# Kernel tuning notes

Measured on AMD Instinct MI355X. Metric: run time of the kernel, lower is better.

The kernel has to match this reference:

```python
import jax, jax.numpy as jnp
import numpy as np

NEG_SLOPE = 0.2  # PyG GATConv default

def gat_conv(x, src, dst, W, att_src, att_dst, bias, n_nodes):
    """PyG-style GATConv (self-loops already included in src/dst)."""
    H, C = att_src.shape
    h = (x @ W).reshape(n_nodes, H, C)                       # [N,H,C]
    a_src = jnp.einsum('nhc,hc->nh', h, att_src)             # [N,H]
    a_dst = jnp.einsum('nhc,hc->nh', h, att_dst)             # [N,H]
    e = jax.nn.leaky_relu(a_src[src] + a_dst[dst], NEG_SLOPE)  # [E,H]
    # numerically stable segment softmax over incoming edges of each dst node
    e_max = jax.ops.segment_max(e, dst, num_segments=n_nodes)   # [N,H]
    e_exp = jnp.exp(e - e_max[dst])
    denom = jax.ops.segment_sum(e_exp, dst, num_segments=n_nodes)  # [N,H]
    alpha = e_exp / (denom[dst] + 1e-16)                     # [E,H]
    msg = h[src] * alpha[:, :, None]                         # [E,H,C]
    out = jax.ops.segment_sum(msg, dst, num_segments=n_nodes)  # [N,H,C]
    return out.reshape(n_nodes, H * C) + bias

def add_self_loops(edge_index, n_nodes):
    loop = jnp.arange(n_nodes, dtype=edge_index.dtype)
    src = jnp.concatenate([edge_index[0], loop])
    dst = jnp.concatenate([edge_index[1], loop])
    return src, dst

def setup_inputs() -> dict:
    key = jax.random.key(0)
    ks = jax.random.split(key, 12)
    N, E, IN, HID, H1 = 50000, 800000, 128, 64, 4
    s = lambda k, shape, scale: jax.random.normal(k, shape, dtype=jnp.float32) * scale
    return {
        'x': s(ks[0], (N, IN), 1.0),
        'edge_index': jax.random.randint(ks[1], (2, E), 0, N, dtype=jnp.int64),
        'W1': s(ks[2], (IN, H1 * HID), (2.0 / IN) ** 0.5),
        'att_src1': s(ks[3], (H1, HID), 0.1),
        'att_dst1': s(ks[4], (H1, HID), 0.1),
        'b1': s(ks[5], (H1 * HID,), 0.02),
        'W2': s(ks[6], (H1 * HID, HID), (2.0 / (H1 * HID)) ** 0.5),
        'att_src2': s(ks[7], (1, HID), 0.1),
        'att_dst2': s(ks[8], (1, HID), 0.1),
        'b2': s(ks[9], (HID,), 0.02),
        'Ws': s(ks[10], (HID, 1), (2.0 / HID) ** 0.5),
        'bs': s(ks[11], (1,), 0.02),
    }

def reference(x, edge_index, W1, att_src1, att_dst1, b1, W2, att_src2, att_dst2, b2, Ws, bs):
    N = x.shape[0]
    src, dst = add_self_loops(edge_index, N)
    h = jax.nn.elu(gat_conv(x, src, dst, W1, att_src1, att_dst1, b1, N))   # [N,256]
    # dropout is identity in eval mode
    h = jax.nn.elu(gat_conv(h, src, dst, W2, att_src2, att_dst2, b2, N))   # [N,64]
    scores = (h @ Ws + bs).squeeze(-1)                                     # [N]
    return h, scores
```

## Files before the change

kernel.cpp:

```cpp
#include <hip/hip_runtime.h>
#include <hip/hip_bf16.h>
#include <math.h>


#define LRELU_SLOPE 0.2f

typedef __attribute__((ext_vector_type(8))) short short8;
typedef __attribute__((ext_vector_type(4))) float f32x4;

__device__ inline ushort f2bf(float f) {
    uint u = __float_as_uint(f);
    return (ushort)((u + 0x7FFFu + ((u >> 16) & 1u)) >> 16);
}
__device__ inline float bf2f(ushort u) {
    return __uint_as_float(((uint)u) << 16);
}

__global__ __launch_bounds__(256)
void prefrag(const float* __restrict__ W, ushort* __restrict__ out,
             int J, int T, int ldn)
{
    int tid = blockIdx.x * blockDim.x + threadIdx.x;
    if (tid >= J * T * 64) return;
    int l = tid & 63, jt = tid >> 6;
    int t = jt % T, j = jt / T;
    int n = j * 16 + (l & 15);
    int k0 = t * 32 + (l >> 4) * 8;
    ushort o[8];
    #pragma unroll
    for (int b = 0; b < 8; ++b) o[b] = f2bf(W[(size_t)(k0 + b) * ldn + n]);
    *(short8*)(out + (size_t)tid * 8) = *(short8*)o;
}

template<int J, int T, int H, bool AF32>
__global__ __launch_bounds__(256)
void gemm_mfma(const void* __restrict__ Araw, const ushort* __restrict__ Bf,
               ushort* __restrict__ Cbf, const float* __restrict__ attS,
               const float* __restrict__ attD, float* __restrict__ as_,
               float* __restrict__ ad_, int M)
{
    constexpr int K = 32 * T;
    constexpr int NN = 16 * J;
    const int l = threadIdx.x & 63;
    const int wid = blockIdx.x * (blockDim.x >> 6) + (threadIdx.x >> 6);
    const int base = wid * 16;
    if (base >= M) return;
    const int lm = l & 15, lg = l >> 4;

    short8 a[T];
    if constexpr (AF32) {
        const float* ap = (const float*)Araw + (size_t)(base + lm) * K + lg * 8;
        #pragma unroll
        for (int t = 0; t < T; ++t) {
            float4 v0 = *(const float4*)(ap + t * 32);
            float4 v1 = *(const float4*)(ap + t * 32 + 4);
            ushort o[8];
            o[0] = f2bf(v0.x); o[1] = f2bf(v0.y); o[2] = f2bf(v0.z); o[3] = f2bf(v0.w);
            o[4] = f2bf(v1.x); o[5] = f2bf(v1.y); o[6] = f2bf(v1.z); o[7] = f2bf(v1.w);
            a[t] = *(short8*)o;
        }
    } else {
        const ushort* ap = (const ushort*)Araw + (size_t)(base + lm) * K + lg * 8;
        #pragma unroll
        for (int t = 0; t < T; ++t) a[t] = *(const short8*)(ap + t * 32);
    }

    f32x4 acc[J];
    #pragma unroll
    for (int j = 0; j < J; ++j) acc[j] = (f32x4){0.f, 0.f, 0.f, 0.f};

    const ushort* bp = Bf + (size_t)l * 8;
    #pragma unroll
    for (int j = 0; j < J; ++j)
        #pragma unroll
        for (int t = 0; t < T; ++t) {
            short8 b = *(const short8*)(bp + (size_t)(j * T + t) * 512);
            acc[j] = __builtin_amdgcn_mfma_f32_16x16x32_bf16(a[t], b, acc[j], 0, 0, 0);
        }

    float sp[H][4], dp[H][4];
    #pragma unroll
    for (int h = 0; h < H; ++h)
        #pragma unroll
        for (int r = 0; r < 4; ++r) { sp[h][r] = 0.f; dp[h][r] = 0.f; }

    #pragma unroll
    for (int j = 0; j < J; ++j) {
        const int h = j / (J / H);
        const int coff = (j % (J / H)) * 16 + lm;
        float ws = attS[h * 64 + coff];
        float wd = attD[h * 64 + coff];
        #pragma unroll
        for (int r = 0; r < 4; ++r) {
            int row = base + lg * 4 + r;
            Cbf[(size_t)row * NN + j * 16 + lm] = f2bf(acc[j][r]);
            sp[h][r] = fmaf(acc[j][r], ws, sp[h][r]);
            dp[h][r] = fmaf(acc[j][r], wd, dp[h][r]);
        }
    }
    #pragma unroll
    for (int h = 0; h < H; ++h)
        #pragma unroll
        for (int r = 0; r < 4; ++r) {
            float s = sp[h][r], d = dp[h][r];
            s += __shfl_xor(s, 1); d += __shfl_xor(d, 1);
            s += __shfl_xor(s, 2); d += __shfl_xor(d, 2);
            s += __shfl_xor(s, 4); d += __shfl_xor(d, 4);
            s += __shfl_xor(s, 8); d += __shfl_xor(d, 8);
            if (lm == 0) {
                int row = base + lg * 4 + r;
                as_[row * H + h] = s;
                ad_[row * H + h] = d;
            }
        }
}

__global__ __launch_bounds__(256)
void degree_hist(const int* __restrict__ edst, int* __restrict__ deg, int E)
{
    int i = blockIdx.x * blockDim.x + threadIdx.x;
    if (i < E) atomicAdd(&deg[edst[i]], 1);
}

__global__ __launch_bounds__(1024)
void scan_rowptr(const int* __restrict__ deg, int* __restrict__ rowptr,
                 int* __restrict__ cursor, int N)
{
    __shared__ int wsums[16];
    __shared__ int s_carry;
    const int tid = threadIdx.x, lane = tid & 63, wid = tid >> 6;
    if (tid == 0) s_carry = 0;
    __syncthreads();
    const int N4 = N >> 2;
    for (int base = 0; base < N4; base += 1024) {
        int i4 = base + tid;
        int4 v = (i4 < N4) ? ((const int4*)deg)[i4] : make_int4(0, 0, 0, 0);
        int tsum = v.x + v.y + v.z + v.w;
        int sc = tsum;
        #pragma unroll
        for (int off = 1; off < 64; off <<= 1) {
            int t = __shfl_up(sc, off);
            if (lane >= off) sc += t;
        }
        if (lane == 63) wsums[wid] = sc;
        __syncthreads();
        if (wid == 0) {
            int wv = (lane < 16) ? wsums[lane] : 0;
            #pragma unroll
            for (int off = 1; off < 16; off <<= 1) {
                int t = __shfl_up(wv, off);
                if (lane >= off) wv += t;
            }
            if (lane < 16) wsums[lane] = wv;
        }
        __syncthreads();
        int wbase = (wid > 0) ? wsums[wid - 1] : 0;
        int excl = s_carry + wbase + sc - tsum;
        if (i4 < N4) {
            int4 o;
            o.x = excl; o.y = excl + v.x; o.z = o.y + v.y; o.w = o.z + v.z;
            ((int4*)rowptr)[i4] = o;
            ((int4*)cursor)[i4] = make_int4(0, 0, 0, 0);
        }
        __syncthreads();
        if (tid == 0) s_carry += wsums[15];
        __syncthreads();
    }
    if (tid == 0) rowptr[N] = s_carry;
}

__global__ __launch_bounds__(256)
void scatter_edges(const int* __restrict__ esrc, const int* __restrict__ edst,
                   const int* __restrict__ rowptr, int* __restrict__ cursor,
                   int* __restrict__ csr_src, int* __restrict__ csr_dst, int E)
{
    int i = blockIdx.x * blockDim.x + threadIdx.x;
    if (i >= E) return;
    int s = esrc[i], d = edst[i];
    int pos = rowptr[d] + atomicAdd(&cursor[d], 1);
    csr_src[pos] = s;
    csr_dst[pos] = d;
}

__global__ __launch_bounds__(256)
void edge_coef_l1(const int* __restrict__ csr_src, const int* __restrict__ csr_dst,
                  const float* __restrict__ as_, const float* __restrict__ ad_,
                  float* __restrict__ p1, int E)
{
    int i = blockIdx.x * blockDim.x + threadIdx.x;
    if (i >= E) return;
    int s = csr_src[i], d = csr_dst[i];
    float4 a = *(const float4*)(as_ + (size_t)s * 4);
    float4 b = *(const float4*)(ad_ + (size_t)d * 4);
    float4 o;
    float e0 = a.x + b.x; e0 = e0 > 0.f ? e0 : LRELU_SLOPE * e0; o.x = __expf(e0);
    float e1 = a.y + b.y; e1 = e1 > 0.f ? e1 : LRELU_SLOPE * e1; o.y = __expf(e1);
    float e2 = a.z + b.z; e2 = e2 > 0.f ? e2 : LRELU_SLOPE * e2; o.z = __expf(e2);
    float e3 = a.w + b.w; e3 = e3 > 0.f ? e3 : LRELU_SLOPE * e3; o.w = __expf(e3);
    *(float4*)(p1 + (size_t)i * 4) = o;
}

__global__ __launch_bounds__(256)
void edge_coef_l2(const int* __restrict__ csr_src, const int* __restrict__ csr_dst,
                  const float* __restrict__ as_, const float* __restrict__ ad_,
                  float* __restrict__ p2, int E)
{
    int i = blockIdx.x * blockDim.x + threadIdx.x;
    if (i >= E) return;
    float e0 = as_[csr_src[i]] + ad_[csr_dst[i]];
    e0 = e0 > 0.f ? e0 : LRELU_SLOPE * e0;
    p2[i] = __expf(e0);
}

__global__ __launch_bounds__(256)
void aggregate_l1(const int* __restrict__ rowptr, const int* __restrict__ csr_src,
                  const float* __restrict__ p1, const ushort* __restrict__ h1,
                  const float* __restrict__ as_, const float* __restrict__ ad_,
                  const float* __restrict__ bias, ushort* __restrict__ outbf, int N)
{
    int w = (blockIdx.x * blockDim.x + threadIdx.x) >> 6;
    int lane = threadIdx.x & 63;
    if (w >= N) return;
    const int head = lane >> 4;
    const int c0 = lane << 2;
    float4 acc;
    float dsum;

    {
        float el = as_[w * 4 + head] + ad_[w * 4 + head];
        el = el > 0.f ? el : LRELU_SLOPE * el;
        float p = __expf(el);
        ushort4 u = *(const ushort4*)(h1 + (size_t)w * 256 + c0);
        acc.x = p * bf2f(u.x); acc.y = p * bf2f(u.y);
        acc.z = p * bf2f(u.z); acc.w = p * bf2f(u.w);
        dsum = p;
    }

    int e = rowptr[w];
    const int e1 = rowptr[w + 1];
    for (; e + 3 < e1; e += 4) {
        int s0 = csr_src[e],     s1 = csr_src[e + 1];
        int s2 = csr_src[e + 2], s3 = csr_src[e + 3];
        float p0 = p1[(size_t)(e + 0) * 4 + head];
        float p1v = p1[(size_t)(e + 1) * 4 + head];
        float p2 = p1[(size_t)(e + 2) * 4 + head];
        float p3 = p1[(size_t)(e + 3) * 4 + head];
        ushort4 u0 = *(const ushort4*)(h1 + (size_t)s0 * 256 + c0);
        ushort4 u1 = *(const ushort4*)(h1 + (size_t)s1 * 256 + c0);
        ushort4 u2 = *(const ushort4*)(h1 + (size_t)s2 * 256 + c0);
        ushort4 u3 = *(const ushort4*)(h1 + (size_t)s3 * 256 + c0);
        acc.x = fmaf(p0, bf2f(u0.x), acc.x); acc.y = fmaf(p0, bf2f(u0.y), acc.y);
        acc.z = fmaf(p0, bf2f(u0.z), acc.z); acc.w = fmaf(p0, bf2f(u0.w), acc.w);
        acc.x = fmaf(p1v, bf2f(u1.x), acc.x); acc.y = fmaf(p1v, bf2f(u1.y), acc.y);
        acc.z = fmaf(p1v, bf2f(u1.z), acc.z); acc.w = fmaf(p1v, bf2f(u1.w), acc.w);
        acc.x = fmaf(p2, bf2f(u2.x), acc.x); acc.y = fmaf(p2, bf2f(u2.y), acc.y);
        acc.z = fmaf(p2, bf2f(u2.z), acc.z); acc.w = fmaf(p2, bf2f(u2.w), acc.w);
        acc.x = fmaf(p3, bf2f(u3.x), acc.x); acc.y = fmaf(p3, bf2f(u3.y), acc.y);
        acc.z = fmaf(p3, bf2f(u3.z), acc.z); acc.w = fmaf(p3, bf2f(u3.w), acc.w);
        dsum += (p0 + p1v) + (p2 + p3);
    }
    for (; e < e1; ++e) {
        int s0 = csr_src[e];
        float p0 = p1[(size_t)e * 4 + head];
        ushort4 u0 = *(const ushort4*)(h1 + (size_t)s0 * 256 + c0);
        acc.x = fmaf(p0, bf2f(u0.x), acc.x); acc.y = fmaf(p0, bf2f(u0.y), acc.y);
        acc.z = fmaf(p0, bf2f(u0.z), acc.z); acc.w = fmaf(p0, bf2f(u0.w), acc.w);
        dsum += p0;
    }
    const float inv = 1.f / (dsum + 1e-16f);
    const float4 b = *(const float4*)(bias + c0);
    float ox = acc.x * inv + b.x; ox = ox > 0.f ? ox : expm1f(ox);
    float oy = acc.y * inv + b.y; oy = oy > 0.f ? oy : expm1f(oy);
    float oz = acc.z * inv + b.z; oz = oz > 0.f ? oz : expm1f(oz);
    float ow = acc.w * inv + b.w; ow = ow > 0.f ? ow : expm1f(ow);
    ushort4 o;
    o.x = f2bf(ox); o.y = f2bf(oy); o.z = f2bf(oz); o.w = f2bf(ow);
    *(ushort4*)(outbf + (size_t)w * 256 + c0) = o;
}

__global__ __launch_bounds__(256)
void aggregate_l2(const int* __restrict__ rowptr, const int* __restrict__ csr_src,
                  const float* __restrict__ p2, const ushort* __restrict__ h2,
                  const float* __restrict__ as_, const float* __restrict__ ad_,
                  const float* __restrict__ b2, const float* __restrict__ Wsv,
                  const float* __restrict__ bs, float* __restrict__ hout,
                  float* __restrict__ scores, int N)
{
    int w = (blockIdx.x * blockDim.x + threadIdx.x) >> 6;
    int lane = threadIdx.x & 63;
    if (w >= N) return;
    float acc, dsum;
    {
        float el = as_[w] + ad_[w];
        el = el > 0.f ? el : LRELU_SLOPE * el;
        float p = __expf(el);
        acc = p * bf2f(h2[(size_t)w * 64 + lane]);
        dsum = p;
    }
    int e = rowptr[w];
    const int e1 = rowptr[w + 1];
    for (; e + 3 < e1; e += 4) {
        int s0 = csr_src[e],     s1 = csr_src[e + 1];
        int s2 = csr_src[e + 2], s3 = csr_src[e + 3];
        float p0 = p2[e], p1 = p2[e + 1], p2v = p2[e + 2], p3 = p2[e + 3];
        acc = fmaf(p0, bf2f(h2[(size_t)s0 * 64 + lane]), acc);
        acc = fmaf(p1, bf2f(h2[(size_t)s1 * 64 + lane]), acc);
        acc = fmaf(p2v, bf2f(h2[(size_t)s2 * 64 + lane]), acc);
        acc = fmaf(p3, bf2f(h2[(size_t)s3 * 64 + lane]), acc);
        dsum += (p0 + p1) + (p2v + p3);
    }
    for (; e < e1; ++e) {
        int s0 = csr_src[e];
        float p0 = p2[e];
        acc = fmaf(p0, bf2f(h2[(size_t)s0 * 64 + lane]), acc);
        dsum += p0;
    }
    float v = acc / (dsum + 1e-16f) + b2[lane];
    v = v > 0.f ? v : expm1f(v);
    hout[(size_t)w * 64 + lane] = v;
    float sc = v * Wsv[lane];
    #pragma unroll
    for (int off = 32; off; off >>= 1) sc += __shfl_down(sc, off);
    if (lane == 0) scores[w] = sc + bs[0];
}

extern "C" void kernel_launch(void* const* d_in, const int* in_sizes, int n_in,
                              void* d_out, int out_size, void* d_ws, size_t ws_size,
                              hipStream_t stream)
{
    const float* x    = (const float*)d_in[0];
    const int*   ei   = (const int*)d_in[1];
    const float* W1   = (const float*)d_in[2];
    const float* as1w = (const float*)d_in[3];
    const float* ad1w = (const float*)d_in[4];
    const float* b1   = (const float*)d_in[5];
    const float* W2   = (const float*)d_in[6];
    const float* as2w = (const float*)d_in[7];
    const float* ad2w = (const float*)d_in[8];
    const float* b2   = (const float*)d_in[9];
    const float* Ws   = (const float*)d_in[10];
    const float* bs   = (const float*)d_in[11];

    const int N  = in_sizes[0] / 128;
    const int E  = in_sizes[1] / 2;
    const int* esrc = ei;
    const int* edst = ei + E;

    ushort* h1bf  = (ushort*)d_ws;
    ushort* hl1bf = h1bf + (size_t)N * 256;
    ushort* h2bf  = hl1bf + (size_t)N * 256;
    ushort* bfr1  = h2bf + (size_t)N * 64;
    ushort* bfr2  = bfr1 + 32768;
    float*  as1   = (float*)(bfr2 + 16384);
    float*  ad1   = as1 + (size_t)N * 4;
    float*  as2   = ad1 + (size_t)N * 4;
    float*  ad2   = as2 + N;
    float*  p1    = ad2 + N;
    float*  p2    = p1 + (size_t)E * 4;
    int*    deg    = (int*)(p2 + E);
    int*    cursor = deg + N;
    int*    rowptr = cursor + N;
    int*    csr_src= rowptr + N + 4;
    int*    csr_dst= csr_src + E;

    float* hout   = (float*)d_out;
    float* scores = hout + (size_t)N * 64;

    hipMemsetAsync(deg, 0, (size_t)N * sizeof(int), stream);
    degree_hist<<<(E + 255) / 256, 256, 0, stream>>>(edst, deg, E);
    scan_rowptr<<<1, 1024, 0, stream>>>(deg, rowptr, cursor, N);
    scatter_edges<<<(E + 255) / 256, 256, 0, stream>>>(
        esrc, edst, rowptr, cursor, csr_src, csr_dst, E);

    prefrag<<<(16 * 4 * 64 + 255) / 256, 256, 0, stream>>>(W1, bfr1, 16, 4, 256);
    prefrag<<<(4 * 8 * 64 + 255) / 256, 256, 0, stream>>>(W2, bfr2, 4, 8, 64);

    gemm_mfma<16, 4, 4, true><<<(N / 16 + 3) / 4, 256, 0, stream>>>(
        x, bfr1, h1bf, as1w, ad1w, as1, ad1, N);
    edge_coef_l1<<<(E + 255) / 256, 256, 0, stream>>>(
        csr_src, csr_dst, as1, ad1, p1, E);
    aggregate_l1<<<((size_t)N * 64 + 255) / 256, 256, 0, stream>>>(
        rowptr, csr_src, p1, h1bf, as1, ad1, b1, hl1bf, N);

    gemm_mfma<4, 8, 1, false><<<(N / 16 + 3) / 4, 256, 0, stream>>>(
        hl1bf, bfr2, h2bf, as2w, ad2w, as2, ad2, N);
    edge_coef_l2<<<(E + 255) / 256, 256, 0, stream>>>(
        csr_src, csr_dst, as2, ad2, p2, E);
    aggregate_l2<<<((size_t)N * 64 + 255) / 256, 256, 0, stream>>>(
        rowptr, csr_src, p2, h2bf, as2, ad2, b2, Ws, bs, hout, scores, N);
}
```

Baseline: 266.2 us.

## Split wavefront across multiple edges per iteration in GAT aggregation kernels

Both aggregation kernels now process several incoming edges at once per wavefront. The lanes are split into half-waves (layer 1, 16-byte loads per lane) or quarter-waves (layer 2, 8-byte loads), each handling a different edge, and the partial sums are combined with cross-lane shuffles at the end. The goal is more independent gathers in flight and wider per-lane loads, to hide gather latency on short adjacency lists. In exchange, the tail iterations do masked, redundant loads, the shuffle reductions add overhead, and some lanes do duplicate epilogue work.

```diff
diff --git a/kernel.cpp b/kernel.cpp
--- a/kernel.cpp
+++ b/kernel.cpp
@@ -221,61 +221,60 @@
     int w = (blockIdx.x * blockDim.x + threadIdx.x) >> 6;
     int lane = threadIdx.x & 63;
     if (w >= N) return;
-    const int head = lane >> 4;
-    const int c0 = lane << 2;
-    float4 acc;
+    const int half = lane >> 5;
+    const int hl   = lane & 31;
+    const int c0   = hl << 3;
+    const int head = hl >> 3;
+
+    float acc[8];
     float dsum;
-
     {
         float el = as_[w * 4 + head] + ad_[w * 4 + head];
         el = el > 0.f ? el : LRELU_SLOPE * el;
-        float p = __expf(el);
-        ushort4 u = *(const ushort4*)(h1 + (size_t)w * 256 + c0);
-        acc.x = p * bf2f(u.x); acc.y = p * bf2f(u.y);
-        acc.z = p * bf2f(u.z); acc.w = p * bf2f(u.w);
+        float p = half ? 0.f : __expf(el);
+        ushort u8[8];
+        *(short8*)u8 = *(const short8*)(h1 + (size_t)w * 256 + c0);
+        #pragma unroll
+        for (int k = 0; k < 8; ++k) acc[k] = p * bf2f(u8[k]);
         dsum = p;
     }
 
     int e = rowptr[w];
     const int e1 = rowptr[w + 1];
-    for (; e + 3 < e1; e += 4) {
-        int s0 = csr_src[e],     s1 = csr_src[e + 1];
-        int s2 = csr_src[e + 2], s3 = csr_src[e + 3];
-        float p0 = p1[(size_t)(e + 0) * 4 + head];
-        float p1v = p1[(size_t)(e + 1) * 4 + head];
-        float p2 = p1[(size_t)(e + 2) * 4 + head];
-        float p3 = p1[(size_t)(e + 3) * 4 + head];
-        ushort4 u0 = *(const ushort4*)(h1 + (size_t)s0 * 256 + c0);
-        ushort4 u1 = *(const ushort4*)(h1 + (size_t)s1 * 256 + c0);
-        ushort4 u2 = *(const ushort4*)(h1 + (size_t)s2 * 256 + c0);
-        ushort4 u3 = *(const ushort4*)(h1 + (size_t)s3 * 256 + c0);
-        acc.x = fmaf(p0, bf2f(u0.x), acc.x); acc.y = fmaf(p0, bf2f(u0.y), acc.y);
-        acc.z = fmaf(p0, bf2f(u0.z), acc.z); acc.w = fmaf(p0, bf2f(u0.w), acc.w);
-        acc.x = fmaf(p1v, bf2f(u1.x), acc.x); acc.y = fmaf(p1v, bf2f(u1.y), acc.y);
-        acc.z = fmaf(p1v, bf2f(u1.z), acc.z); acc.w = fmaf(p1v, bf2f(u1.w), acc.w);
-        acc.x = fmaf(p2, bf2f(u2.x), acc.x); acc.y = fmaf(p2, bf2f(u2.y), acc.y);
-        acc.z = fmaf(p2, bf2f(u2.z), acc.z); acc.w = fmaf(p2, bf2f(u2.w), acc.w);
-        acc.x = fmaf(p3, bf2f(u3.x), acc.x); acc.y = fmaf(p3, bf2f(u3.y), acc.y);
-        acc.z = fmaf(p3, bf2f(u3.z), acc.z); acc.w = fmaf(p3, bf2f(u3.w), acc.w);
-        dsum += (p0 + p1v) + (p2 + p3);
-    }
-    for (; e < e1; ++e) {
-        int s0 = csr_src[e];
-        float p0 = p1[(size_t)e * 4 + head];
-        ushort4 u0 = *(const ushort4*)(h1 + (size_t)s0 * 256 + c0);
-        acc.x = fmaf(p0, bf2f(u0.x), acc.x); acc.y = fmaf(p0, bf2f(u0.y), acc.y);
-        acc.z = fmaf(p0, bf2f(u0.z), acc.z); acc.w = fmaf(p0, bf2f(u0.w), acc.w);
-        dsum += p0;
-    }
+    const int eL = e1 - 1;
+    while (e < e1) {
+        #pragma unroll
+        for (int u = 0; u < 4; ++u) {
+            int m = e + 2 * u + half;
+            int idx = m <= eL ? m : eL;
+            int s = csr_src[idx];
+            float p = m <= eL ? p1[(size_t)idx * 4 + head] : 0.f;
+            ushort u8[8];
+            *(short8*)u8 = *(const short8*)(h1 + (size_t)s * 256 + c0);
+            #pragma unroll
+            for (int k = 0; k < 8; ++k) acc[k] = fmaf(p, bf2f(u8[k]), acc[k]);
+            dsum += p;
+        }
+        e += 8;
+    }
+
+    dsum += __shfl_xor(dsum, 32);
+    #pragma unroll
+    for (int k = 0; k < 8; ++k) acc[k] += __shfl_xor(acc[k], 32);
+
     const float inv = 1.f / (dsum + 1e-16f);
-    const float4 b = *(const float4*)(bias + c0);
-    float ox = acc.x * inv + b.x; ox = ox > 0.f ? ox : expm1f(ox);
-    float oy = acc.y * inv + b.y; oy = oy > 0.f ? oy : expm1f(oy);
-    float oz = acc.z * inv + b.z; oz = oz > 0.f ? oz : expm1f(oz);
-    float ow = acc.w * inv + b.w; ow = ow > 0.f ? ow : expm1f(ow);
-    ushort4 o;
-    o.x = f2bf(ox); o.y = f2bf(oy); o.z = f2bf(oz); o.w = f2bf(ow);
-    *(ushort4*)(outbf + (size_t)w * 256 + c0) = o;
+    const float4 b0 = *(const float4*)(bias + c0);
+    const float4 b1 = *(const float4*)(bias + c0 + 4);
+    float bb[8] = {b0.x, b0.y, b0.z, b0.w, b1.x, b1.y, b1.z, b1.w};
+    ushort o[8];
+    #pragma unroll
+    for (int k = 0; k < 8; ++k) {
+        float v = acc[k] * inv + bb[k];
+        v = v > 0.f ? v : expm1f(v);
+        o[k] = f2bf(v);
+    }
+    if (half == 0)
+        *(short8*)(outbf + (size_t)w * 256 + c0) = *(short8*)o;
 }
 
 __global__ __launch_bounds__(256)
@@ -289,38 +288,61 @@
     int w = (blockIdx.x * blockDim.x + threadIdx.x) >> 6;
     int lane = threadIdx.x & 63;
     if (w >= N) return;
-    float acc, dsum;
+    const int q  = lane >> 4;
+    const int ql = lane & 15;
+    const int c0 = ql << 2;
+
+    float acc[4];
+    float dsum;
     {
         float el = as_[w] + ad_[w];
         el = el > 0.f ? el : LRELU_SLOPE * el;
-        float p = __expf(el);
-        acc = p * bf2f(h2[(size_t)w * 64 + lane]);
+        float p = (q == 0) ? __expf(el) : 0.f;
+        ushort u4[4];
+        *(ushort4*)u4 = *(const ushort4*)(h2 + (size_t)w * 64 + c0);
+        #pragma unroll
+        for (int k = 0; k < 4; ++k) acc[k] = p * bf2f(u4[k]);
         dsum = p;
     }
+
     int e = rowptr[w];
     const int e1 = rowptr[w + 1];
-    for (; e + 3 < e1; e += 4) {
-        int s0 = csr_src[e],     s1 = csr_src[e + 1];
-        int s2 = csr_src[e + 2], s3 = csr_src[e + 3];
-        float p0 = p2[e], p1 = p2[e + 1], p2v = p2[e + 2], p3 = p2[e + 3];
-        acc = fmaf(p0, bf2f(h2[(size_t)s0 * 64 + lane]), acc);
-        acc = fmaf(p1, bf2f(h2[(size_t)s1 * 64 + lane]), acc);
-        acc = fmaf(p2v, bf2f(h2[(size_t)s2 * 64 + lane]), acc);
-        acc = fmaf(p3, bf2f(h2[(size_t)s3 * 64 + lane]), acc);
-        dsum += (p0 + p1) + (p2v + p3);
-    }
-    for (; e < e1; ++e) {
-        int s0 = csr_src[e];
-        float p0 = p2[e];
-        acc = fmaf(p0, bf2f(h2[(size_t)s0 * 64 + lane]), acc);
-        dsum += p0;
-    }
-    float v = acc / (dsum + 1e-16f) + b2[lane];
-    v = v > 0.f ? v : expm1f(v);
-    hout[(size_t)w * 64 + lane] = v;
-    float sc = v * Wsv[lane];
-    #pragma unroll
-    for (int off = 32; off; off >>= 1) sc += __shfl_down(sc, off);
+    const int eL = e1 - 1;
+    while (e < e1) {
+        #pragma unroll
+        for (int u = 0; u < 2; ++u) {
+            int m = e + 4 * u + q;
+            int idx = m <= eL ? m : eL;
+            int s = csr_src[idx];
+            float p = m <= eL ? p2[idx] : 0.f;
+            ushort u4[4];
+            *(ushort4*)u4 = *(const ushort4*)(h2 + (size_t)s * 64 + c0);
+            #pragma unroll
+            for (int k = 0; k < 4; ++k) acc[k] = fmaf(p, bf2f(u4[k]), acc[k]);
+            dsum += p;
+        }
+        e += 8;
+    }
+
+    dsum += __shfl_xor(dsum, 16); dsum += __shfl_xor(dsum, 32);
+    #pragma unroll
+    for (int k = 0; k < 4; ++k) {
+        acc[k] += __shfl_xor(acc[k], 16);
+        acc[k] += __shfl_xor(acc[k], 32);
+    }
+
+    const float inv = 1.f / (dsum + 1e-16f);
+    const float4 bb = *(const float4*)(b2 + c0);
+    const float4 ww = *(const float4*)(Wsv + c0);
+    float v0 = acc[0] * inv + bb.x; v0 = v0 > 0.f ? v0 : expm1f(v0);
+    float v1 = acc[1] * inv + bb.y; v1 = v1 > 0.f ? v1 : expm1f(v1);
+    float v2 = acc[2] * inv + bb.z; v2 = v2 > 0.f ? v2 : expm1f(v2);
+    float v3 = acc[3] * inv + bb.w; v3 = v3 > 0.f ? v3 : expm1f(v3);
+    if (q == 0)
+        *(float4*)(hout + (size_t)w * 64 + c0) = make_float4(v0, v1, v2, v3);
+    float sc = fmaf(v0, ww.x, fmaf(v1, ww.y, fmaf(v2, ww.z, v3 * ww.w)));
+    sc += __shfl_xor(sc, 1); sc += __shfl_xor(sc, 2);
+    sc += __shfl_xor(sc, 4); sc += __shfl_xor(sc, 8);
     if (lane == 0) scores[w] = sc + bs[0];
 }
 
```

After: 278.6 us. +4.6%, slower.

## Drop csr_dst and cursor, use node-centric edge coefficients, single-pass scan

Applied to the files above, without the earlier changes.

Removes the csr_dst array by computing edge coefficients per destination node from rowptr, and reuses the degree array as a decrementing cursor so the cursor buffer and its zeroing go away. The rowptr scan becomes a single pass with 13 int4 chunks per thread instead of a looped block scan. Degree histogram loads four indices per thread, and the two weight-prefragment launches are merged into one. Node-centric coefficient kernels may leave many lanes idle for low-degree nodes, and the scan now assumes N fits in 1024*52 entries.

```diff
diff --git a/kernel.cpp b/kernel.cpp
--- a/kernel.cpp
+++ b/kernel.cpp
@@ -16,12 +16,10 @@
     return __uint_as_float(((uint)u) << 16);
 }
 
-__global__ __launch_bounds__(256)
-void prefrag(const float* __restrict__ W, ushort* __restrict__ out,
-             int J, int T, int ldn)
-{
-    int tid = blockIdx.x * blockDim.x + threadIdx.x;
-    if (tid >= J * T * 64) return;
+__device__ inline void prefrag_one(const float* __restrict__ W,
+                                   ushort* __restrict__ out,
+                                   int tid, int T, int ldn)
+{
     int l = tid & 63, jt = tid >> 6;
     int t = jt % T, j = jt / T;
     int n = j * 16 + (l & 15);
@@ -30,6 +28,16 @@
     #pragma unroll
     for (int b = 0; b < 8; ++b) o[b] = f2bf(W[(size_t)(k0 + b) * ldn + n]);
     *(short8*)(out + (size_t)tid * 8) = *(short8*)o;
+}
+
+__global__ __launch_bounds__(256)
+void prefrag_both(const float* __restrict__ W1, const float* __restrict__ W2,
+                  ushort* __restrict__ o1, ushort* __restrict__ o2)
+{
+    int tid = blockIdx.x * blockDim.x + threadIdx.x;
+    if (tid < 16 * 4 * 64)             prefrag_one(W1, o1, tid, 4, 256);
+    else if (tid < 16 * 4 * 64 + 4 * 8 * 64)
+        prefrag_one(W2, o2, tid - 16 * 4 * 64, 8, 64);
 }
 
 template<int J, int T, int H, bool AF32>
@@ -118,98 +126,112 @@
 __global__ __launch_bounds__(256)
 void degree_hist(const int* __restrict__ edst, int* __restrict__ deg, int E)
 {
-    int i = blockIdx.x * blockDim.x + threadIdx.x;
-    if (i < E) atomicAdd(&deg[edst[i]], 1);
+    int i = (blockIdx.x * blockDim.x + threadIdx.x) << 2;
+    if (i + 3 < E) {
+        int4 v = *(const int4*)(edst + i);
+        atomicAdd(&deg[v.x], 1); atomicAdd(&deg[v.y], 1);
+        atomicAdd(&deg[v.z], 1); atomicAdd(&deg[v.w], 1);
+    } else {
+        for (; i < E; ++i) atomicAdd(&deg[edst[i]], 1);
+    }
 }
 
 __global__ __launch_bounds__(1024)
-void scan_rowptr(const int* __restrict__ deg, int* __restrict__ rowptr,
-                 int* __restrict__ cursor, int N)
+void scan_rowptr(const int* __restrict__ deg, int* __restrict__ rowptr, int N)
 {
     __shared__ int wsums[16];
-    __shared__ int s_carry;
     const int tid = threadIdx.x, lane = tid & 63, wid = tid >> 6;
-    if (tid == 0) s_carry = 0;
+    const int N4 = N >> 2;
+    const int b4 = tid * 13;
+    int tsum = 0;
+    #pragma unroll
+    for (int k = 0; k < 13; ++k) {
+        int i4 = b4 + k;
+        if (i4 < N4) {
+            int4 v = ((const int4*)deg)[i4];
+            tsum += (v.x + v.y) + (v.z + v.w);
+        }
+    }
+    int sc = tsum;
+    #pragma unroll
+    for (int off = 1; off < 64; off <<= 1) {
+        int t = __shfl_up(sc, off);
+        if (lane >= off) sc += t;
+    }
+    if (lane == 63) wsums[wid] = sc;
     __syncthreads();
-    const int N4 = N >> 2;
-    for (int base = 0; base < N4; base += 1024) {
-        int i4 = base + tid;
-        int4 v = (i4 < N4) ? ((const int4*)deg)[i4] : make_int4(0, 0, 0, 0);
-        int tsum = v.x + v.y + v.z + v.w;
-        int sc = tsum;
-        #pragma unroll
-        for (int off = 1; off < 64; off <<= 1) {
-            int t = __shfl_up(sc, off);
-            if (lane >= off) sc += t;
-        }
-        if (lane == 63) wsums[wid] = sc;
-        __syncthreads();
-        if (wid == 0) {
-            int wv = (lane < 16) ? wsums[lane] : 0;
-            #pragma unroll
-            for (int off = 1; off < 16; off <<= 1) {
-                int t = __shfl_up(wv, off);
-                if (lane >= off) wv += t;
-            }
-            if (lane < 16) wsums[lane] = wv;
-        }
-        __syncthreads();
-        int wbase = (wid > 0) ? wsums[wid - 1] : 0;
-        int excl = s_carry + wbase + sc - tsum;
+    if (wid == 0) {
+        int wv = (lane < 16) ? wsums[lane] : 0;
+        #pragma unroll
+        for (int off = 1; off < 16; off <<= 1) {
+            int t = __shfl_up(wv, off);
+            if (lane >= off) wv += t;
+        }
+        if (lane < 16) wsums[lane] = wv;
+    }
+    __syncthreads();
+    int run = (wid ? wsums[wid - 1] : 0) + sc - tsum;
+    #pragma unroll
+    for (int k = 0; k < 13; ++k) {
+        int i4 = b4 + k;
         if (i4 < N4) {
+            int4 v = ((const int4*)deg)[i4];
             int4 o;
-            o.x = excl; o.y = excl + v.x; o.z = o.y + v.y; o.w = o.z + v.z;
+            o.x = run; o.y = run + v.x; o.z = o.y + v.y; o.w = o.z + v.z;
             ((int4*)rowptr)[i4] = o;
-            ((int4*)cursor)[i4] = make_int4(0, 0, 0, 0);
-        }
-        __syncthreads();
-        if (tid == 0) s_carry += wsums[15];
-        __syncthreads();
-    }
-    if (tid == 0) rowptr[N] = s_carry;
+            run += (v.x + v.y) + (v.z + v.w);
+        }
+    }
+    if (tid == 1023) rowptr[N] = run;
 }
 
 __global__ __launch_bounds__(256)
 void scatter_edges(const int* __restrict__ esrc, const int* __restrict__ edst,
-                   const int* __restrict__ rowptr, int* __restrict__ cursor,
-                   int* __restrict__ csr_src, int* __restrict__ csr_dst, int E)
+                   const int* __restrict__ rowptr, int* __restrict__ deg,
+                   int* __restrict__ csr_src, int E)
 {
     int i = blockIdx.x * blockDim.x + threadIdx.x;
     if (i >= E) return;
     int s = esrc[i], d = edst[i];
-    int pos = rowptr[d] + atomicAdd(&cursor[d], 1);
+    int pos = rowptr[d] + atomicSub(&deg[d], 1) - 1;
     csr_src[pos] = s;
-    csr_dst[pos] = d;
-}
-
-__global__ __launch_bounds__(256)
-void edge_coef_l1(const int* __restrict__ csr_src, const int* __restrict__ csr_dst,
+}
+
+__global__ __launch_bounds__(256)
+void edge_coef_l1(const int* __restrict__ rowptr, const int* __restrict__ csr_src,
                   const float* __restrict__ as_, const float* __restrict__ ad_,
-                  float* __restrict__ p1, int E)
-{
-    int i = blockIdx.x * blockDim.x + threadIdx.x;
-    if (i >= E) return;
-    int s = csr_src[i], d = csr_dst[i];
-    float4 a = *(const float4*)(as_ + (size_t)s * 4);
-    float4 b = *(const float4*)(ad_ + (size_t)d * 4);
-    float4 o;
-    float e0 = a.x + b.x; e0 = e0 > 0.f ? e0 : LRELU_SLOPE * e0; o.x = __expf(e0);
-    float e1 = a.y + b.y; e1 = e1 > 0.f ? e1 : LRELU_SLOPE * e1; o.y = __expf(e1);
-    float e2 = a.z + b.z; e2 = e2 > 0.f ? e2 : LRELU_SLOPE * e2; o.z = __expf(e2);
-    float e3 = a.w + b.w; e3 = e3 > 0.f ? e3 : LRELU_SLOPE * e3; o.w = __expf(e3);
-    *(float4*)(p1 + (size_t)i * 4) = o;
-}
-
-__global__ __launch_bounds__(256)
-void edge_coef_l2(const int* __restrict__ csr_src, const int* __restrict__ csr_dst,
+                  float* __restrict__ p1, int N)
+{
+    int w = (blockIdx.x * blockDim.x + threadIdx.x) >> 6;
+    int lane = threadIdx.x & 63;
+    if (w >= N) return;
+    const int head = lane & 3;
+    const int slot = lane >> 2;
+    const float adv = ad_[w * 4 + head];
+    const int e1 = rowptr[w + 1];
+    for (int c = rowptr[w] + slot; c < e1; c += 16) {
+        int s = csr_src[c];
+        float e = as_[s * 4 + head] + adv;
+        e = e > 0.f ? e : LRELU_SLOPE * e;
+        p1[(size_t)c * 4 + head] = __expf(e);
+    }
+}
+
+__global__ __launch_bounds__(256)
+void edge_coef_l2(const int* __restrict__ rowptr, const int* __restrict__ csr_src,
                   const float* __restrict__ as_, const float* __restrict__ ad_,
-                  float* __restrict__ p2, int E)
-{
-    int i = blockIdx.x * blockDim.x + threadIdx.x;
-    if (i >= E) return;
-    float e0 = as_[csr_src[i]] + ad_[csr_dst[i]];
-    e0 = e0 > 0.f ? e0 : LRELU_SLOPE * e0;
-    p2[i] = __expf(e0);
+                  float* __restrict__ p2, int N)
+{
+    int w = (blockIdx.x * blockDim.x + threadIdx.x) >> 6;
+    int lane = threadIdx.x & 63;
+    if (w >= N) return;
+    const float adv = ad_[w];
+    const int e1 = rowptr[w + 1];
+    for (int c = rowptr[w] + lane; c < e1; c += 64) {
+        float e = as_[csr_src[c]] + adv;
+        e = e > 0.f ? e : LRELU_SLOPE * e;
+        p2[c] = __expf(e);
+    }
 }
 
 __global__ __launch_bounds__(256)
@@ -358,34 +380,32 @@
     float*  p1    = ad2 + N;
     float*  p2    = p1 + (size_t)E * 4;
     int*    deg    = (int*)(p2 + E);
-    int*    cursor = deg + N;
-    int*    rowptr = cursor + N;
+    int*    rowptr = deg + N;
     int*    csr_src= rowptr + N + 4;
-    int*    csr_dst= csr_src + E;
 
     float* hout   = (float*)d_out;
     float* scores = hout + (size_t)N * 64;
 
     hipMemsetAsync(deg, 0, (size_t)N * sizeof(int), stream);
-    degree_hist<<<(E + 255) / 256, 256, 0, stream>>>(edst, deg, E);
-    scan_rowptr<<<1, 1024, 0, stream>>>(deg, rowptr, cursor, N);
+    degree_hist<<<(E / 4 + 255) / 256, 256, 0, stream>>>(edst, deg, E);
+    scan_rowptr<<<1, 1024, 0, stream>>>(deg, rowptr, N);
     scatter_edges<<<(E + 255) / 256, 256, 0, stream>>>(
-        esrc, edst, rowptr, cursor, csr_src, csr_dst, E);
-
-    prefrag<<<(16 * 4 * 64 + 255) / 256, 256, 0, stream>>>(W1, bfr1, 16, 4, 256);
-    prefrag<<<(4 * 8 * 64 + 255) / 256, 256, 0, stream>>>(W2, bfr2, 4, 8, 64);
+        esrc, edst, rowptr, deg, csr_src, E);
+
+    prefrag_both<<<(16 * 4 * 64 + 4 * 8 * 64 + 255) / 256, 256, 0, stream>>>(
+        W1, W2, bfr1, bfr2);
 
     gemm_mfma<16, 4, 4, true><<<(N / 16 + 3) / 4, 256, 0, stream>>>(
         x, bfr1, h1bf, as1w, ad1w, as1, ad1, N);
-    edge_coef_l1<<<(E + 255) / 256, 256, 0, stream>>>(
-        csr_src, csr_dst, as1, ad1, p1, E);
+    edge_coef_l1<<<((size_t)N * 64 + 255) / 256, 256, 0, stream>>>(
+        rowptr, csr_src, as1, ad1, p1, N);
     aggregate_l1<<<((size_t)N * 64 + 255) / 256, 256, 0, stream>>>(
         rowptr, csr_src, p1, h1bf, as1, ad1, b1, hl1bf, N);
 
     gemm_mfma<4, 8, 1, false><<<(N / 16 + 3) / 4, 256, 0, stream>>>(
         hl1bf, bfr2, h2bf, as2w, ad2w, as2, ad2, N);
-    edge_coef_l2<<<(E + 255) / 256, 256, 0, stream>>>(
-        csr_src, csr_dst, as2, ad2, p2, E);
+    edge_coef_l2<<<((size_t)N * 64 + 255) / 256, 256, 0, stream>>>(
+        rowptr, csr_src, as2, ad2, p2, N);
     aggregate_l2<<<((size_t)N * 64 + 255) / 256, 256, 0, stream>>>(
         rowptr, csr_src, p2, h2bf, as2, ad2, b2, Ws, bs, hout, scores, N);
 }
```

Result: slower. 283.7 us (+6.6%).
